# Kernel optimization log

Measured on AMD Instinct MI355X. Metric: run time of the kernel, lower is better.

## Reference

```python
import jax, jax.numpy as jnp
import numpy as np
from jax import lax

N = 20000          # num_nodes_total
N_GHOST = 2000     # nodes with mask == 0
T_IN = 8
FEAT = 16          # node_features
HID = 128          # hidden_dim
E = 320000         # edges (~avg degree 16)
D = 2              # downstream_concat_depth
ALPHA = 0.5        # alpha_boundary
FUSER_IN = FEAT * (1 + D) + 1   # 49
FUSER_H = max(32, 2 * FEAT * (1 + D))  # 96
GATE_H = max(8, FUSER_H // 2)   # 48


def _lin(k, fan_in, shape):
    b = 1.0 / np.sqrt(fan_in)
    return jax.random.uniform(k, shape, jnp.float32, -b, b)


def setup_inputs() -> dict:
    key = jax.random.key(0)
    ks = jax.random.split(key, 26)
    x = jax.random.normal(ks[0], (N, T_IN, FEAT), jnp.float32)
    src = jax.random.randint(ks[1], (E,), 0, N, jnp.int32)
    dst = jax.random.randint(ks[2], (E,), 0, N, jnp.int32)
    # guarantee every ghost node (ids [0, N_GHOST)) has an outgoing edge to a real node
    src = src.at[:N_GHOST].set(jnp.arange(N_GHOST, dtype=jnp.int32))
    dst = dst.at[:N_GHOST].set(jax.random.randint(ks[3], (N_GHOST,), N_GHOST, N, jnp.int32))
    edge_index = jnp.stack([src, dst])
    edge_attr = jax.random.uniform(ks[4], (E, 1), jnp.float32, minval=0.05, maxval=2.0)
    mask = jnp.concatenate([jnp.zeros(N_GHOST, jnp.int32), jnp.ones(N - N_GHOST, jnp.int32)])
    H3 = 3 * HID
    return dict(
        x=x, edge_attr=edge_attr,
        W_lin=_lin(ks[5], FEAT, (FEAT, HID)), b_lin=_lin(ks[6], FEAT, (HID,)),
        Wc1=_lin(ks[7], HID, (HID, HID)), bc1=jnp.zeros((HID,), jnp.float32),
        Wc2=_lin(ks[8], HID, (HID, HID)), bc2=jnp.zeros((HID,), jnp.float32),
        W_ih=_lin(ks[9], HID, (HID, H3)), b_ih=_lin(ks[10], HID, (H3,)),
        W_hh=_lin(ks[11], HID, (HID, H3)), b_hh=_lin(ks[12], HID, (H3,)),
        Wf1=_lin(ks[13], FUSER_IN, (FUSER_IN, FUSER_H)), bf1=_lin(ks[14], FUSER_IN, (FUSER_H,)),
        Wf2=_lin(ks[15], FUSER_H, (FUSER_H, FEAT)), bf2=_lin(ks[16], FUSER_H, (FEAT,)),
        Wg1=_lin(ks[17], FUSER_IN, (FUSER_IN, GATE_H)), bg1=_lin(ks[18], FUSER_IN, (GATE_H,)),
        Wg2=_lin(ks[19], GATE_H, (GATE_H, 1)), bg2=_lin(ks[20], GATE_H, (1,)),
        edge_index=edge_index, mask=mask,
    )


def _forward(x, edge_attr, W_lin, b_lin, Wc1, bc1, Wc2, bc2, W_ih, b_ih, W_hh, b_hh,
             Wf1, bf1, Wf2, bf2, Wg1, bg1, Wg2, bg2, edge_index, mask):
    src, dst = edge_index[0], edge_index[1]
    ghost_idx = jnp.nonzero(mask == 0, size=N_GHOST)[0]
    dist = jnp.maximum(edge_attr[:, 0], 1e-6)                     # [E]
    # first outgoing edge per source node (earliest edge id per src, cf. argsort trick)
    eid = jnp.arange(E, dtype=jnp.int32)
    first_eid = jax.ops.segment_min(eid, src, num_segments=N)    # int32 max where no edge
    has = first_eid < E
    safe = jnp.where(has, first_eid, 0)
    first_out = jnp.where(has, dst[safe], -1)                     # [N]
    first_dx = jnp.where(has, dist[safe], -1.0)                   # [N]
    b_idx = first_out[ghost_idx]                                  # boundary node per ghost
    dx_bnd = jnp.maximum(first_dx[ghost_idx], 1e-6)[:, None]      # [G,1]
    # D downstream hops, staying put where no outgoing edge exists
    dK, cur = [], b_idx
    for _ in range(D):
        nxt = first_out[cur]
        nxt = jnp.where(nxt < 0, cur, nxt)
        dK.append(nxt)
        cur = nxt
    # GCN symmetric normalization with self-loops (PyG gcn_norm)
    deg = jnp.zeros((N,), x.dtype).at[dst].add(1.0) + 1.0         # in-degree + self-loop
    dis = deg ** -0.5
    norm_e = (dis[src] * dis[dst])[:, None]                       # [E,1]
    norm_self = (1.0 / deg)[:, None]                              # [N,1]

    def gcn(h, W, b):
        hw = h @ W                                                # [N,HID]
        agg = jnp.zeros_like(hw).at[dst].add(hw[src] * norm_e)    # scatter-add messages
        return agg + hw * norm_self + b

    def gru(g, h):
        gi = g @ W_ih + b_ih                                      # [N,3H]
        gh = h @ W_hh + b_hh
        ir, iz, inn = jnp.split(gi, 3, axis=1)
        hr, hz, hn = jnp.split(gh, 3, axis=1)
        r = jax.nn.sigmoid(ir + hr)
        z = jax.nn.sigmoid(iz + hz)
        n = jnp.tanh(inn + r * hn)
        return (1.0 - z) * n + z * h

    def step(h, x_t):
        gf = x_t[ghost_idx]                                       # [G,F]
        feats = jnp.concatenate([gf] + [x_t[i] for i in dK] + [dx_bnd], axis=1)  # [G,FUSER_IN]
        zf = jax.nn.relu(feats @ Wf1 + bf1)
        delta = zf @ Wf2 + bf2
        gate = jax.nn.sigmoid(jax.nn.relu(feats @ Wg1 + bg1) @ Wg2 + bg2)
        x_t = x_t.at[ghost_idx].set(gf + ALPHA * delta * gate)
        g = jax.nn.relu(x_t @ W_lin + b_lin)
        g = jax.nn.relu(gcn(g, Wc1, bc1))
        g = jax.nn.relu(gcn(g, Wc2, bc2))
        return gru(g, h), None

    h0 = jnp.zeros((N, HID), x.dtype)
    h, _ = lax.scan(step, h0, jnp.swapaxes(x, 0, 1))              # scan over T_IN
    return h


def reference(x, edge_attr, W_lin, b_lin, Wc1, bc1, Wc2, bc2, W_ih, b_ih, W_hh, b_hh,
              Wf1, bf1, Wf2, bf2, Wg1, bg1, Wg2, bg2, edge_index, mask):
    return _forward(x, edge_attr, W_lin, b_lin, Wc1, bc1, Wc2, bc2, W_ih, b_ih, W_hh, b_hh,
                    Wf1, bf1, Wf2, bf2, Wg1, bg1, Wg2, bg2, edge_index, mask)
```

## Files before the change

### kernel.cpp

```cpp
#include <hip/hip_runtime.h>
#include <math.h>

#define NN 20000
#define T_IN 8
#define FEAT 16
#define HID 128
#define H3 384
#define FUSER_IN 49
#define FUSER_H 96
#define GATE_H 48
#define ALPHA 0.5f

typedef unsigned short u16;
typedef __attribute__((ext_vector_type(8))) short bf16x8_t;
typedef __attribute__((ext_vector_type(4))) float f32x4_t;

__device__ __forceinline__ float sigmoidf_(float v) { return 1.0f / (1.0f + expf(-v)); }

__device__ __forceinline__ u16 f2b(float v) {
    unsigned u = __float_as_uint(v);
    unsigned r = (u + 0x7fffu + ((u >> 16) & 1u)) >> 16;
    return (u16)r;
}
__device__ __forceinline__ float b2f(u16 u) { return __uint_as_float(((unsigned)u) << 16); }


__global__ void init_kernel(int* first_eid, int* deg_cnt, int* gcount, int n) {
    int i = blockIdx.x * 256 + threadIdx.x;
    if (i < n) { first_eid[i] = 0x7fffffff; deg_cnt[i] = 0; }
    if (i == 0) *gcount = 0;
}

__global__ void edge_pass1(const int* __restrict__ src, const int* __restrict__ dst,
                           int* first_eid, int* deg_cnt, int e) {
    int i = blockIdx.x * 256 + threadIdx.x;
    if (i < e) {
        atomicMin(&first_eid[src[i]], i);
        atomicAdd(&deg_cnt[dst[i]], 1);
    }
}

__global__ void scan1(const int* __restrict__ cnt, int* tmp, int* bsum, int n) {
    __shared__ int buf[256];
    int tid = threadIdx.x;
    int i = blockIdx.x * 256 + tid;
    int v = (i < n) ? cnt[i] : 0;
    buf[tid] = v;
    __syncthreads();
    #pragma unroll
    for (int off = 1; off < 256; off <<= 1) {
        int t = (tid >= off) ? buf[tid - off] : 0;
        __syncthreads();
        buf[tid] += t;
        __syncthreads();
    }
    if (i < n) tmp[i] = buf[tid];
    if (tid == 255) bsum[blockIdx.x] = buf[255];
}

__global__ void scan2(int* bsum, int nb) {
    __shared__ int buf[256];
    int tid = threadIdx.x;
    int v = (tid < nb) ? bsum[tid] : 0;
    buf[tid] = v;
    __syncthreads();
    #pragma unroll
    for (int off = 1; off < 256; off <<= 1) {
        int t = (tid >= off) ? buf[tid - off] : 0;
        __syncthreads();
        buf[tid] += t;
        __syncthreads();
    }
    if (tid < nb) bsum[tid] = buf[tid];
}

__global__ void scan3(const int* __restrict__ cnt, const int* __restrict__ tmp,
                      const int* __restrict__ bsum,
                      int* row_ptr, int* fill_ptr, float* dis, float* norm_self, int n) {
    int i = blockIdx.x * 256 + threadIdx.x;
    if (i >= n) return;
    int pre = (blockIdx.x > 0) ? bsum[blockIdx.x - 1] : 0;
    int incl = tmp[i] + pre;
    int v = cnt[i];
    row_ptr[i + 1] = incl;
    fill_ptr[i] = incl - v;
    float deg = (float)v + 1.0f;
    dis[i] = 1.0f / sqrtf(deg);
    norm_self[i] = 1.0f / deg;
    if (i == 0) row_ptr[0] = 0;
}

__global__ void firsts_kernel(const int* __restrict__ first_eid, const int* __restrict__ dst,
                              const float* __restrict__ edge_attr,
                              int* first_out, float* first_dx, int n, int e) {
    int i = blockIdx.x * 256 + threadIdx.x;
    if (i >= n) return;
    int fe = first_eid[i];
    if (fe < e) {
        first_out[i] = dst[fe];
        first_dx[i] = fmaxf(edge_attr[fe], 1e-6f);
    } else {
        first_out[i] = -1;
        first_dx[i] = -1.0f;
    }
}

__global__ void edge_pass2(const int* __restrict__ src, const int* __restrict__ dst,
                           int* fill_ptr, const float* __restrict__ dis,
                           int* csr_src, float* csr_w, int e) {
    int i = blockIdx.x * 256 + threadIdx.x;
    if (i < e) {
        int d = dst[i], s = src[i];
        int pos = atomicAdd(&fill_ptr[d], 1);
        csr_src[pos] = s;
        csr_w[pos] = dis[s] * dis[d];
    }
}

__global__ void ghost_kernel(const int* __restrict__ mask, const int* __restrict__ first_out,
                             const float* __restrict__ first_dx,
                             int* d1_of, int* d2_of, float* dxb_of,
                             int* ghost_list, int* ghost_pos, int* gcount, int n) {
    int i = blockIdx.x * 256 + threadIdx.x;
    if (i >= n) return;
    if (mask[i] != 0) { ghost_pos[i] = -1; return; }
    int pos = atomicAdd(gcount, 1);
    ghost_list[pos] = i;
    ghost_pos[i] = pos;
    int b = first_out[i];
    float dxb = fmaxf(first_dx[i], 1e-6f);
    int d1, d2;
    if (b < 0) { d1 = i; d2 = i; }
    else {
        int n1 = first_out[b]; d1 = (n1 < 0) ? b : n1;
        int n2 = first_out[d1]; d2 = (n2 < 0) ? d1 : n2;
    }
    d1_of[i] = d1; d2_of[i] = d2; dxb_of[i] = dxb;
}

__global__ void zero2_kernel(float* a, int na, unsigned* b, int nb) {
    int stride = gridDim.x * 256;
    for (int i = blockIdx.x * 256 + threadIdx.x; i < na; i += stride) a[i] = 0.0f;
    for (int i = blockIdx.x * 256 + threadIdx.x; i < nb; i += stride) b[i] = 0u;
}

__global__ __launch_bounds__(256)
void wsplit_kernel(const float* __restrict__ W, u16* BT_hi, u16* BT_lo, int Ncols) {
    __shared__ float tile[32][33];
    int nb = blockIdx.x * 32;
    int kb = blockIdx.y * 32;
    int tx = threadIdx.x & 31, ty = threadIdx.x >> 5;
    #pragma unroll
    for (int r = 0; r < 32; r += 8)
        tile[ty + r][tx] = W[(size_t)(kb + ty + r) * Ncols + nb + tx];
    __syncthreads();
    #pragma unroll
    for (int r = 0; r < 32; r += 8) {
        float v = tile[tx][ty + r];
        u16 h = f2b(v);
        size_t off = (size_t)(nb + ty + r) * 128 + kb + tx;
        BT_hi[off] = h;
        BT_lo[off] = f2b(v - b2f(h));
    }
}


__global__ __launch_bounds__(128)
void fuse_ghost(const float* __restrict__ x,
                const int* __restrict__ ghost_list, const int* __restrict__ gcount,
                const int* __restrict__ d1_of, const int* __restrict__ d2_of,
                const float* __restrict__ dxb_of,
                const float* __restrict__ Wf1, const float* __restrict__ bf1,
                const float* __restrict__ Wf2, const float* __restrict__ bf2,
                const float* __restrict__ Wg1, const float* __restrict__ bg1,
                const float* __restrict__ Wg2, const float* __restrict__ bg2,
                float* __restrict__ xf_buf) {
    int slot = blockIdx.x;
    if (slot >= *gcount) return;
    int t = blockIdx.y;
    int i = ghost_list[slot];
    int j = threadIdx.x;
    __shared__ float feats[FUSER_IN];
    __shared__ float z1[FUSER_H];
    __shared__ float zg[GATE_H];
    __shared__ float s_gate;

    if (j < FEAT) {
        int d1 = d1_of[i], d2 = d2_of[i];
        feats[j]            = x[((size_t)i * T_IN + t) * FEAT + j];
        feats[FEAT + j]     = x[((size_t)d1 * T_IN + t) * FEAT + j];
        feats[2 * FEAT + j] = x[((size_t)d2 * T_IN + t) * FEAT + j];
    }
    if (j == 0) feats[3 * FEAT] = dxb_of[i];
    __syncthreads();
    if (j < FUSER_H) {
        float acc = bf1[j];
        for (int k = 0; k < FUSER_IN; ++k) acc = fmaf(feats[k], Wf1[k * FUSER_H + j], acc);
        z1[j] = fmaxf(acc, 0.0f);
    }
    if (j < GATE_H) {
        float acc = bg1[j];
        for (int k = 0; k < FUSER_IN; ++k) acc = fmaf(feats[k], Wg1[k * GATE_H + j], acc);
        zg[j] = fmaxf(acc, 0.0f);
    }
    __syncthreads();
    if (j == 0) {
        float s = bg2[0];
        for (int k = 0; k < GATE_H; ++k) s = fmaf(zg[k], Wg2[k], s);
        s_gate = sigmoidf_(s);
    }
    __syncthreads();
    if (j < FEAT) {
        float acc = bf2[j];
        for (int k = 0; k < FUSER_H; ++k) acc = fmaf(z1[k], Wf2[k * FEAT + j], acc);
        xf_buf[((size_t)slot * T_IN + t) * FEAT + j] = feats[j] + ALPHA * acc * s_gate;
    }
}

__global__ __launch_bounds__(256)
void lin_all(const float* __restrict__ x, const float* __restrict__ xf_buf,
             const int* __restrict__ ghost_pos,
             const float* __restrict__ W_lin, const float* __restrict__ b_lin,
             u16* __restrict__ g8_hi, u16* __restrict__ g8_lo, int n, int total) {
    __shared__ float Wl[FEAT][HID];
    __shared__ float bl[HID];
    #pragma unroll
    for (int k8 = 0; k8 < 8; ++k8) {
        int idx = threadIdx.x + k8 * 256;
        Wl[idx >> 7][idx & 127] = W_lin[idx];
    }
    if (threadIdx.x < HID) bl[threadIdx.x] = b_lin[threadIdx.x];
    __syncthreads();
    int j = threadIdx.x & 127;
    for (int pair = blockIdx.x * 2 + (threadIdx.x >> 7); pair < total; pair += gridDim.x * 2) {
        int node = pair % n;
        int t = pair / n;
        int gp = ghost_pos[node];
        const float* xr = (gp >= 0) ? &xf_buf[((size_t)gp * T_IN + t) * FEAT]
                                    : &x[((size_t)node * T_IN + t) * FEAT];
        float acc = bl[j];
        #pragma unroll
        for (int k = 0; k < FEAT; ++k) acc = fmaf(xr[k], Wl[k][j], acc);
        float v = fmaxf(acc, 0.0f);
        u16 hv = f2b(v);
        size_t off = (size_t)pair * HID + j;
        g8_hi[off] = hv;
        g8_lo[off] = f2b(v - b2f(hv));
    }
}

__global__ __launch_bounds__(256)
void gemm_gcn_b(const u16* __restrict__ Ahi0, const u16* __restrict__ Alo0,
                const u16* __restrict__ BThi, const u16* __restrict__ BTlo,
                u16* __restrict__ Cb0, int M) {
    constexpr int BM = 64;
    __shared__ u16 ldsA[2][BM * 128];
    const size_t tOff = (size_t)blockIdx.z * M * 128;
    const u16* Ahi = Ahi0 + tOff;
    const u16* Alo = Alo0 + tOff;
    u16*       Cb  = Cb0 + tOff;

    const int tid  = threadIdx.x;
    const int row0 = blockIdx.x * BM;
    constexpr int MF = BM / 32;

    #pragma unroll
    for (int it = 0; it < BM / 16; ++it) {
        int unit = tid + it * 256;
        int r = unit >> 4, s = unit & 15;
        int gr = row0 + r;
        uint4 vh = make_uint4(0, 0, 0, 0), vl = vh;
        if (gr < M) {
            vh = *reinterpret_cast<const uint4*>(&Ahi[(size_t)gr * 128 + s * 8]);
            vl = *reinterpret_cast<const uint4*>(&Alo[(size_t)gr * 128 + s * 8]);
        }
        int byte = (r * 256 + s * 16) ^ ((r & 7) << 4);
        *reinterpret_cast<uint4*>((char*)(&ldsA[0][0]) + byte) = vh;
        *reinterpret_cast<uint4*>((char*)(&ldsA[1][0]) + byte) = vl;
    }
    __syncthreads();

    const int wid  = tid >> 6;
    const int lane = tid & 63;
    const int wr = (wid >> 1) * (BM / 2);
    const int wc = (wid & 1) * 64;
    const int l15 = lane & 15;
    const int lkh = lane >> 4;

    f32x4_t acc[MF][4] = {};

    #pragma unroll
    for (int kb = 0; kb < 4; ++kb) {
        bf16x8_t ah[MF], al[MF], bh[4], bl[4];
        #pragma unroll
        for (int m = 0; m < MF; ++m) {
            int row = wr + m * 16 + l15;
            int byte = (row * 256 + kb * 64 + lkh * 16) ^ ((row & 7) << 4);
            ah[m] = *reinterpret_cast<const bf16x8_t*>((const char*)(&ldsA[0][0]) + byte);
            al[m] = *reinterpret_cast<const bf16x8_t*>((const char*)(&ldsA[1][0]) + byte);
        }
        #pragma unroll
        for (int nf = 0; nf < 4; ++nf) {
            int col = wc + nf * 16 + l15;
            size_t off = (size_t)col * 128 + kb * 32 + lkh * 8;
            bh[nf] = *reinterpret_cast<const bf16x8_t*>(&BThi[off]);
            bl[nf] = *reinterpret_cast<const bf16x8_t*>(&BTlo[off]);
        }
        #pragma unroll
        for (int m = 0; m < MF; ++m)
            #pragma unroll
            for (int nf = 0; nf < 4; ++nf) {
                acc[m][nf] = __builtin_amdgcn_mfma_f32_16x16x32_bf16(ah[m], bh[nf], acc[m][nf], 0, 0, 0);
                acc[m][nf] = __builtin_amdgcn_mfma_f32_16x16x32_bf16(ah[m], bl[nf], acc[m][nf], 0, 0, 0);
                acc[m][nf] = __builtin_amdgcn_mfma_f32_16x16x32_bf16(al[m], bh[nf], acc[m][nf], 0, 0, 0);
            }
    }

    #pragma unroll
    for (int m = 0; m < MF; ++m) {
        int rbase = row0 + wr + m * 16 + lkh * 4;
        #pragma unroll
        for (int nf = 0; nf < 4; ++nf) {
            int col = wc + nf * 16 + l15;
            #pragma unroll
            for (int r2 = 0; r2 < 4; ++r2) {
                int row = rbase + r2;
                if (row < M) Cb[(size_t)row * 128 + col] = f2b(acc[m][nf][r2]);
            }
        }
    }
}

__global__ __launch_bounds__(256)
void gcn_agg_b(const u16* __restrict__ hwb0,
               const int* __restrict__ row_ptr,
               const int* __restrict__ csr_src, const float* __restrict__ csr_w,
               const float* __restrict__ norm_self, const float* __restrict__ bias,
               u16* __restrict__ g_hi0, u16* __restrict__ g_lo0, int n) {
    int t   = blockIdx.x & 7;
    int blk = blockIdx.x >> 3;
    int node = blk * 8 + (threadIdx.x >> 5);
    int lane = threadIdx.x & 31;
    if (node >= n) return;
    const size_t tOff = (size_t)t * n * 128;
    const u16* hwb = hwb0 + tOff;
    u16* g_hi = g_hi0 + tOff;
    u16* g_lo = g_lo0 + tOff;

    ushort4 sv = *reinterpret_cast<const ushort4*>(&hwb[(size_t)node * HID + lane * 4]);
    float ns = norm_self[node];
    float4 a0, a1, a2, a3;
    a0.x = b2f(sv.x) * ns; a0.y = b2f(sv.y) * ns; a0.z = b2f(sv.z) * ns; a0.w = b2f(sv.w) * ns;
    a1 = make_float4(0.f, 0.f, 0.f, 0.f); a2 = a1; a3 = a1;
    int p  = row_ptr[node];
    int p1 = row_ptr[node + 1];
    for (; p + 4 <= p1; p += 4) {
        int s0 = csr_src[p], s1 = csr_src[p + 1], s2 = csr_src[p + 2], s3 = csr_src[p + 3];
        float w0 = csr_w[p], w1 = csr_w[p + 1], w2 = csr_w[p + 2], w3 = csr_w[p + 3];
        ushort4 v0 = *reinterpret_cast<const ushort4*>(&hwb[(size_t)s0 * HID + lane * 4]);
        ushort4 v1 = *reinterpret_cast<const ushort4*>(&hwb[(size_t)s1 * HID + lane * 4]);
        ushort4 v2 = *reinterpret_cast<const ushort4*>(&hwb[(size_t)s2 * HID + lane * 4]);
        ushort4 v3 = *reinterpret_cast<const ushort4*>(&hwb[(size_t)s3 * HID + lane * 4]);
        a0.x = fmaf(b2f(v0.x), w0, a0.x); a0.y = fmaf(b2f(v0.y), w0, a0.y);
        a0.z = fmaf(b2f(v0.z), w0, a0.z); a0.w = fmaf(b2f(v0.w), w0, a0.w);
        a1.x = fmaf(b2f(v1.x), w1, a1.x); a1.y = fmaf(b2f(v1.y), w1, a1.y);
        a1.z = fmaf(b2f(v1.z), w1, a1.z); a1.w = fmaf(b2f(v1.w), w1, a1.w);
        a2.x = fmaf(b2f(v2.x), w2, a2.x); a2.y = fmaf(b2f(v2.y), w2, a2.y);
        a2.z = fmaf(b2f(v2.z), w2, a2.z); a2.w = fmaf(b2f(v2.w), w2, a2.w);
        a3.x = fmaf(b2f(v3.x), w3, a3.x); a3.y = fmaf(b2f(v3.y), w3, a3.y);
        a3.z = fmaf(b2f(v3.z), w3, a3.z); a3.w = fmaf(b2f(v3.w), w3, a3.w);
    }
    for (; p < p1; ++p) {
        int s = csr_src[p];
        float w = csr_w[p];
        ushort4 v = *reinterpret_cast<const ushort4*>(&hwb[(size_t)s * HID + lane * 4]);
        a0.x = fmaf(b2f(v.x), w, a0.x); a0.y = fmaf(b2f(v.y), w, a0.y);
        a0.z = fmaf(b2f(v.z), w, a0.z); a0.w = fmaf(b2f(v.w), w, a0.w);
    }
    float4 b4 = reinterpret_cast<const float4*>(bias)[lane];
    float ox = fmaxf(a0.x + a1.x + a2.x + a3.x + b4.x, 0.0f);
    float oy = fmaxf(a0.y + a1.y + a2.y + a3.y + b4.y, 0.0f);
    float oz = fmaxf(a0.z + a1.z + a2.z + a3.z + b4.z, 0.0f);
    float ow = fmaxf(a0.w + a1.w + a2.w + a3.w + b4.w, 0.0f);
    ushort4 hv, lv;
    hv.x = f2b(ox); lv.x = f2b(ox - b2f(hv.x));
    hv.y = f2b(oy); lv.y = f2b(oy - b2f(hv.y));
    hv.z = f2b(oz); lv.z = f2b(oz - b2f(hv.z));
    hv.w = f2b(ow); lv.w = f2b(ow - b2f(hv.w));
    *reinterpret_cast<ushort4*>(&g_hi[(size_t)node * HID + lane * 4]) = hv;
    *reinterpret_cast<ushort4*>(&g_lo[(size_t)node * HID + lane * 4]) = lv;
}


__global__ __launch_bounds__(256)
void gemm_gru(const u16* __restrict__ Ahi1, const u16* __restrict__ Alo1,
              const u16* __restrict__ BThi1, const u16* __restrict__ BTlo1,
              float* __restrict__ C1,
              const u16* __restrict__ Ahi2, const u16* __restrict__ Alo2,
              const u16* __restrict__ BThi2, const u16* __restrict__ BTlo2,
              float* __restrict__ C2,
              int M, int Ncols) {
    constexpr int BM = 128;
    __shared__ u16 ldsA[2][BM * 128];
    const u16* Ahi  = blockIdx.z ? Ahi2  : Ahi1;
    const u16* Alo  = blockIdx.z ? Alo2  : Alo1;
    const u16* BThi = blockIdx.z ? BThi2 : BThi1;
    const u16* BTlo = blockIdx.z ? BTlo2 : BTlo1;
    float*     C    = blockIdx.z ? C2    : C1;

    const int tid  = threadIdx.x;
    const int row0 = blockIdx.x * BM;
    const int col0 = blockIdx.y * 128;
    constexpr int MF = BM / 32;

    #pragma unroll
    for (int it = 0; it < BM / 16; ++it) {
        int unit = tid + it * 256;
        int r = unit >> 4, s = unit & 15;
        int gr = row0 + r;
        uint4 vh = make_uint4(0, 0, 0, 0), vl = vh;
        if (gr < M) {
            vh = *reinterpret_cast<const uint4*>(&Ahi[(size_t)gr * 128 + s * 8]);
            vl = *reinterpret_cast<const uint4*>(&Alo[(size_t)gr * 128 + s * 8]);
        }
        int byte = (r * 256 + s * 16) ^ ((r & 7) << 4);
        *reinterpret_cast<uint4*>((char*)(&ldsA[0][0]) + byte) = vh;
        *reinterpret_cast<uint4*>((char*)(&ldsA[1][0]) + byte) = vl;
    }
    __syncthreads();

    const int wid  = tid >> 6;
    const int lane = tid & 63;
    const int wr = (wid >> 1) * (BM / 2);
    const int wc = (wid & 1) * 64;
    const int l15 = lane & 15;
    const int lkh = lane >> 4;

    f32x4_t acc[MF][4] = {};

    #pragma unroll
    for (int kb = 0; kb < 4; ++kb) {
        bf16x8_t ah[MF], al[MF], bh[4], bl[4];
        #pragma unroll
        for (int m = 0; m < MF; ++m) {
            int row = wr + m * 16 + l15;
            int byte = (row * 256 + kb * 64 + lkh * 16) ^ ((row & 7) << 4);
            ah[m] = *reinterpret_cast<const bf16x8_t*>((const char*)(&ldsA[0][0]) + byte);
            al[m] = *reinterpret_cast<const bf16x8_t*>((const char*)(&ldsA[1][0]) + byte);
        }
        #pragma unroll
        for (int nf = 0; nf < 4; ++nf) {
            int col = col0 + wc + nf * 16 + l15;
            size_t off = (size_t)col * 128 + kb * 32 + lkh * 8;
            bh[nf] = *reinterpret_cast<const bf16x8_t*>(&BThi[off]);
            bl[nf] = *reinterpret_cast<const bf16x8_t*>(&BTlo[off]);
        }
        #pragma unroll
        for (int m = 0; m < MF; ++m)
            #pragma unroll
            for (int nf = 0; nf < 4; ++nf) {
                acc[m][nf] = __builtin_amdgcn_mfma_f32_16x16x32_bf16(ah[m], bh[nf], acc[m][nf], 0, 0, 0);
                acc[m][nf] = __builtin_amdgcn_mfma_f32_16x16x32_bf16(ah[m], bl[nf], acc[m][nf], 0, 0, 0);
                acc[m][nf] = __builtin_amdgcn_mfma_f32_16x16x32_bf16(al[m], bh[nf], acc[m][nf], 0, 0, 0);
            }
    }

    #pragma unroll
    for (int m = 0; m < MF; ++m) {
        int rbase = row0 + wr + m * 16 + lkh * 4;
        #pragma unroll
        for (int nf = 0; nf < 4; ++nf) {
            int col = col0 + wc + nf * 16 + l15;
            #pragma unroll
            for (int r2 = 0; r2 < 4; ++r2) {
                int row = rbase + r2;
                if (row < M) C[(size_t)row * Ncols + col] = acc[m][nf][r2];
            }
        }
    }
}

__global__ __launch_bounds__(256)
void gru_kernel(const float* __restrict__ gi, const float* __restrict__ gh,
                const float* __restrict__ b_ih, const float* __restrict__ b_hh,
                float* __restrict__ h, u16* __restrict__ h_hi, u16* __restrict__ h_lo, int n) {
    int idx = blockIdx.x * 256 + threadIdx.x;
    if (idx >= n * 32) return;
    int row = idx >> 5, q = idx & 31;
    const float4* gi4 = reinterpret_cast<const float4*>(gi + (size_t)row * H3);
    const float4* gh4 = reinterpret_cast<const float4*>(gh + (size_t)row * H3);
    const float4* bi4 = reinterpret_cast<const float4*>(b_ih);
    const float4* bh4 = reinterpret_cast<const float4*>(b_hh);
    float4 vir = gi4[q], viz = gi4[32 + q], vin = gi4[64 + q];
    float4 vhr = gh4[q], vhz = gh4[32 + q], vhn = gh4[64 + q];
    float4 bir = bi4[q], biz = bi4[32 + q], bin_ = bi4[64 + q];
    float4 bhr = bh4[q], bhz = bh4[32 + q], bhn = bh4[64 + q];
    float4* h4 = reinterpret_cast<float4*>(h);
    float4 hv = h4[idx];
    float4 o;
    {
        float r = sigmoidf_((vir.x + bir.x) + (vhr.x + bhr.x));
        float z = sigmoidf_((viz.x + biz.x) + (vhz.x + bhz.x));
        float nn2 = tanhf((vin.x + bin_.x) + r * (vhn.x + bhn.x));
        o.x = (1.0f - z) * nn2 + z * hv.x;
    }
    {
        float r = sigmoidf_((vir.y + bir.y) + (vhr.y + bhr.y));
        float z = sigmoidf_((viz.y + biz.y) + (vhz.y + bhz.y));
        float nn2 = tanhf((vin.y + bin_.y) + r * (vhn.y + bhn.y));
        o.y = (1.0f - z) * nn2 + z * hv.y;
    }
    {
        float r = sigmoidf_((vir.z + bir.z) + (vhr.z + bhr.z));
        float z = sigmoidf_((viz.z + biz.z) + (vhz.z + bhz.z));
        float nn2 = tanhf((vin.z + bin_.z) + r * (vhn.z + bhn.z));
        o.z = (1.0f - z) * nn2 + z * hv.z;
    }
    {
        float r = sigmoidf_((vir.w + bir.w) + (vhr.w + bhr.w));
        float z = sigmoidf_((viz.w + biz.w) + (vhz.w + bhz.w));
        float nn2 = tanhf((vin.w + bin_.w) + r * (vhn.w + bhn.w));
        o.w = (1.0f - z) * nn2 + z * hv.w;
    }
    h4[idx] = o;
    ushort4 hvv, lvv;
    hvv.x = f2b(o.x); lvv.x = f2b(o.x - b2f(hvv.x));
    hvv.y = f2b(o.y); lvv.y = f2b(o.y - b2f(hvv.y));
    hvv.z = f2b(o.z); lvv.z = f2b(o.z - b2f(hvv.z));
    hvv.w = f2b(o.w); lvv.w = f2b(o.w - b2f(hvv.w));
    *reinterpret_cast<ushort4*>(&h_hi[(size_t)row * HID + q * 4]) = hvv;
    *reinterpret_cast<ushort4*>(&h_lo[(size_t)row * HID + q * 4]) = lvv;
}


extern "C" void kernel_launch(void* const* d_in, const int* in_sizes, int n_in,
                              void* d_out, int out_size, void* d_ws, size_t ws_size,
                              hipStream_t stream) {
    const float* x        = (const float*)d_in[0];
    const float* edge_attr= (const float*)d_in[1];
    const float* W_lin    = (const float*)d_in[2];
    const float* b_lin    = (const float*)d_in[3];
    const float* Wc1      = (const float*)d_in[4];
    const float* bc1      = (const float*)d_in[5];
    const float* Wc2      = (const float*)d_in[6];
    const float* bc2      = (const float*)d_in[7];
    const float* W_ih     = (const float*)d_in[8];
    const float* b_ih     = (const float*)d_in[9];
    const float* W_hh     = (const float*)d_in[10];
    const float* b_hh     = (const float*)d_in[11];
    const float* Wf1      = (const float*)d_in[12];
    const float* bf1      = (const float*)d_in[13];
    const float* Wf2      = (const float*)d_in[14];
    const float* bf2      = (const float*)d_in[15];
    const float* Wg1      = (const float*)d_in[16];
    const float* bg1      = (const float*)d_in[17];
    const float* Wg2      = (const float*)d_in[18];
    const float* bg2      = (const float*)d_in[19];
    const int*   edge_index = (const int*)d_in[20];
    const int*   mask     = (const int*)d_in[21];

    const int n = in_sizes[21];
    const int e = in_sizes[1];
    const int* src = edge_index;
    const int* dst = edge_index + e;
    float* h = (float*)d_out;

    char* w = (char*)d_ws;
    auto alloc = [&](size_t bytes) -> char* {
        char* p = w;
        w += (bytes + 255) & ~(size_t)255;
        return p;
    };
    int*   first_eid = (int*)  alloc((size_t)n * 4);
    int*   deg_cnt   = (int*)  alloc((size_t)n * 4);
    int*   row_ptr   = (int*)  alloc((size_t)(n + 1) * 4);
    int*   fill_ptr  = (int*)  alloc((size_t)n * 4);
    int*   tmp_scan  = (int*)  alloc((size_t)n * 4);
    int*   bsum      = (int*)  alloc((size_t)256 * 4);
    float* dis       = (float*)alloc((size_t)n * 4);
    float* norm_self = (float*)alloc((size_t)n * 4);
    int*   first_out = (int*)  alloc((size_t)n * 4);
    float* first_dx  = (float*)alloc((size_t)n * 4);
    int*   d1_of     = (int*)  alloc((size_t)n * 4);
    int*   d2_of     = (int*)  alloc((size_t)n * 4);
    float* dxb_of    = (float*)alloc((size_t)n * 4);
    int*   ghost_list= (int*)  alloc((size_t)n * 4);
    int*   ghost_pos = (int*)  alloc((size_t)n * 4);
    int*   gcount    = (int*)  alloc(256);
    int*   csr_src   = (int*)  alloc((size_t)e * 4);
    float* csr_w     = (float*)alloc((size_t)e * 4);
    u16* Wc1T_hi = (u16*)alloc((size_t)HID * 128 * 2);
    u16* Wc1T_lo = (u16*)alloc((size_t)HID * 128 * 2);
    u16* Wc2T_hi = (u16*)alloc((size_t)HID * 128 * 2);
    u16* Wc2T_lo = (u16*)alloc((size_t)HID * 128 * 2);
    u16* WihT_hi = (u16*)alloc((size_t)H3 * 128 * 2);
    u16* WihT_lo = (u16*)alloc((size_t)H3 * 128 * 2);
    u16* WhhT_hi = (u16*)alloc((size_t)H3 * 128 * 2);
    u16* WhhT_lo = (u16*)alloc((size_t)H3 * 128 * 2);
    u16*   g8_hi = (u16*)  alloc((size_t)T_IN * n * HID * 2);
    u16*   g8_lo = (u16*)  alloc((size_t)T_IN * n * HID * 2);
    u16*   bufHb = (u16*)  alloc((size_t)T_IN * n * HID * 2);
    float* bufGi = (float*)alloc((size_t)n * H3 * 4);
    float* bufGh = (float*)alloc((size_t)n * H3 * 4);
    float* xf_buf= (float*)alloc((size_t)n * T_IN * FEAT * 4);
    u16*   h_hi  = (u16*)  alloc((size_t)n * HID * 2);
    u16*   h_lo  = (u16*)  alloc((size_t)n * HID * 2);

    const int TPB = 256;
    const int nb = (n + 255) / 256;
    dim3 gN(nb), gE((e + TPB - 1) / TPB);

    init_kernel<<<gN, TPB, 0, stream>>>(first_eid, deg_cnt, gcount, n);
    edge_pass1<<<gE, TPB, 0, stream>>>(src, dst, first_eid, deg_cnt, e);
    scan1<<<gN, TPB, 0, stream>>>(deg_cnt, tmp_scan, bsum, n);
    scan2<<<1, TPB, 0, stream>>>(bsum, nb);
    scan3<<<gN, TPB, 0, stream>>>(deg_cnt, tmp_scan, bsum, row_ptr, fill_ptr, dis, norm_self, n);
    firsts_kernel<<<gN, TPB, 0, stream>>>(first_eid, dst, edge_attr, first_out, first_dx, n, e);
    edge_pass2<<<gE, TPB, 0, stream>>>(src, dst, fill_ptr, dis, csr_src, csr_w, e);
    ghost_kernel<<<gN, TPB, 0, stream>>>(mask, first_out, first_dx, d1_of, d2_of, dxb_of,
                                         ghost_list, ghost_pos, gcount, n);
    wsplit_kernel<<<dim3(HID / 32, 4), TPB, 0, stream>>>(Wc1, Wc1T_hi, Wc1T_lo, HID);
    wsplit_kernel<<<dim3(HID / 32, 4), TPB, 0, stream>>>(Wc2, Wc2T_hi, Wc2T_lo, HID);
    wsplit_kernel<<<dim3(H3 / 32, 4), TPB, 0, stream>>>(W_ih, WihT_hi, WihT_lo, H3);
    wsplit_kernel<<<dim3(H3 / 32, 4), TPB, 0, stream>>>(W_hh, WhhT_hi, WhhT_lo, H3);

    zero2_kernel<<<2048, TPB, 0, stream>>>(h, n * HID, (unsigned*)h_hi, n * HID);

    fuse_ghost<<<dim3(n, T_IN), 128, 0, stream>>>(x, ghost_list, gcount, d1_of, d2_of, dxb_of,
                                                  Wf1, bf1, Wf2, bf2, Wg1, bg1, Wg2, bg2,
                                                  xf_buf);
    lin_all<<<2048, 256, 0, stream>>>(x, xf_buf, ghost_pos, W_lin, b_lin,
                                      g8_hi, g8_lo, n, n * T_IN);
    dim3 grid_gcn((n + 63) / 64, 1, T_IN);
    const int agg_blocks = ((n + 7) / 8) * T_IN;
    gemm_gcn_b<<<grid_gcn, 256, 0, stream>>>(g8_hi, g8_lo, Wc1T_hi, Wc1T_lo, bufHb, n);
    gcn_agg_b<<<agg_blocks, 256, 0, stream>>>(bufHb, row_ptr, csr_src, csr_w,
                                              norm_self, bc1, g8_hi, g8_lo, n);
    gemm_gcn_b<<<grid_gcn, 256, 0, stream>>>(g8_hi, g8_lo, Wc2T_hi, Wc2T_lo, bufHb, n);
    gcn_agg_b<<<agg_blocks, 256, 0, stream>>>(bufHb, row_ptr, csr_src, csr_w,
                                              norm_self, bc2, g8_hi, g8_lo, n);

    dim3 grid_gru((n + 127) / 128, 3, 2);
    for (int t = 0; t < T_IN; ++t) {
        const u16* Gt_hi = g8_hi + (size_t)t * n * HID;
        const u16* Gt_lo = g8_lo + (size_t)t * n * HID;
        gemm_gru<<<grid_gru, 256, 0, stream>>>(
            Gt_hi, Gt_lo, WihT_hi, WihT_lo, bufGi,
            h_hi, h_lo, WhhT_hi, WhhT_lo, bufGh, n, H3);
        gru_kernel<<<(n * 32 + TPB - 1) / TPB, TPB, 0, stream>>>(bufGi, bufGh, b_ih, b_hh,
                                                                 h, h_hi, h_lo, n);
    }
}
```

Baseline: 938.0 us.

## Fuse GRU gate GEMMs with the elementwise update and split GCN aggregation by columns

The separate GRU GEMM kernel, which wrote fp32 gate pre-activations for the input and hidden paths to global buffers, and the elementwise GRU kernel that read them back are replaced by one kernel. Each block loads a 32-row tile of the input and hidden state into LDS, computes all three gates for both paths with split-bf16 MFMA, and applies the GRU update in registers. This removes the large per-timestep round trip through the gate buffers, at the cost of each block re-reading the full weight matrices from cache. The GCN aggregation kernel now handles 16 nodes per block with 16 lanes each, and splits the feature columns into two halves across separate blocks, which doubles the block count and shortens each lane's work.

```diff
diff --git a/kernel.cpp b/kernel.cpp
--- a/kernel.cpp
+++ b/kernel.cpp
@@ -336,18 +336,22 @@
                const int* __restrict__ row_ptr,
                const int* __restrict__ csr_src, const float* __restrict__ csr_w,
                const float* __restrict__ norm_self, const float* __restrict__ bias,
-               u16* __restrict__ g_hi0, u16* __restrict__ g_lo0, int n) {
-    int t   = blockIdx.x & 7;
-    int blk = blockIdx.x >> 3;
-    int node = blk * 8 + (threadIdx.x >> 5);
-    int lane = threadIdx.x & 31;
+               u16* __restrict__ g_hi0, u16* __restrict__ g_lo0, int n, int nblk) {
+    int bid = blockIdx.x;
+    int t = bid & 7;
+    int q = bid >> 3;
+    int blk = q % nblk;
+    int half = q / nblk;
+    int node = blk * 16 + (threadIdx.x >> 4);
+    int lane = threadIdx.x & 15;
     if (node >= n) return;
     const size_t tOff = (size_t)t * n * 128;
     const u16* hwb = hwb0 + tOff;
     u16* g_hi = g_hi0 + tOff;
     u16* g_lo = g_lo0 + tOff;
-
-    ushort4 sv = *reinterpret_cast<const ushort4*>(&hwb[(size_t)node * HID + lane * 4]);
+    const int cb = half * 64 + lane * 4;
+
+    ushort4 sv = *reinterpret_cast<const ushort4*>(&hwb[(size_t)node * HID + cb]);
     float ns = norm_self[node];
     float4 a0, a1, a2, a3;
     a0.x = b2f(sv.x) * ns; a0.y = b2f(sv.y) * ns; a0.z = b2f(sv.z) * ns; a0.w = b2f(sv.w) * ns;
@@ -357,10 +361,10 @@
     for (; p + 4 <= p1; p += 4) {
         int s0 = csr_src[p], s1 = csr_src[p + 1], s2 = csr_src[p + 2], s3 = csr_src[p + 3];
         float w0 = csr_w[p], w1 = csr_w[p + 1], w2 = csr_w[p + 2], w3 = csr_w[p + 3];
-        ushort4 v0 = *reinterpret_cast<const ushort4*>(&hwb[(size_t)s0 * HID + lane * 4]);
-        ushort4 v1 = *reinterpret_cast<const ushort4*>(&hwb[(size_t)s1 * HID + lane * 4]);
-        ushort4 v2 = *reinterpret_cast<const ushort4*>(&hwb[(size_t)s2 * HID + lane * 4]);
-        ushort4 v3 = *reinterpret_cast<const ushort4*>(&hwb[(size_t)s3 * HID + lane * 4]);
+        ushort4 v0 = *reinterpret_cast<const ushort4*>(&hwb[(size_t)s0 * HID + cb]);
+        ushort4 v1 = *reinterpret_cast<const ushort4*>(&hwb[(size_t)s1 * HID + cb]);
+        ushort4 v2 = *reinterpret_cast<const ushort4*>(&hwb[(size_t)s2 * HID + cb]);
+        ushort4 v3 = *reinterpret_cast<const ushort4*>(&hwb[(size_t)s3 * HID + cb]);
         a0.x = fmaf(b2f(v0.x), w0, a0.x); a0.y = fmaf(b2f(v0.y), w0, a0.y);
         a0.z = fmaf(b2f(v0.z), w0, a0.z); a0.w = fmaf(b2f(v0.w), w0, a0.w);
         a1.x = fmaf(b2f(v1.x), w1, a1.x); a1.y = fmaf(b2f(v1.y), w1, a1.y);
@@ -373,11 +377,11 @@
     for (; p < p1; ++p) {
         int s = csr_src[p];
         float w = csr_w[p];
-        ushort4 v = *reinterpret_cast<const ushort4*>(&hwb[(size_t)s * HID + lane * 4]);
+        ushort4 v = *reinterpret_cast<const ushort4*>(&hwb[(size_t)s * HID + cb]);
         a0.x = fmaf(b2f(v.x), w, a0.x); a0.y = fmaf(b2f(v.y), w, a0.y);
         a0.z = fmaf(b2f(v.z), w, a0.z); a0.w = fmaf(b2f(v.w), w, a0.w);
     }
-    float4 b4 = reinterpret_cast<const float4*>(bias)[lane];
+    float4 b4 = reinterpret_cast<const float4*>(bias)[half * 16 + lane];
     float ox = fmaxf(a0.x + a1.x + a2.x + a3.x + b4.x, 0.0f);
     float oy = fmaxf(a0.y + a1.y + a2.y + a3.y + b4.y, 0.0f);
     float oz = fmaxf(a0.z + a1.z + a2.z + a3.z + b4.z, 0.0f);
@@ -387,149 +391,111 @@
     hv.y = f2b(oy); lv.y = f2b(oy - b2f(hv.y));
     hv.z = f2b(oz); lv.z = f2b(oz - b2f(hv.z));
     hv.w = f2b(ow); lv.w = f2b(ow - b2f(hv.w));
-    *reinterpret_cast<ushort4*>(&g_hi[(size_t)node * HID + lane * 4]) = hv;
-    *reinterpret_cast<ushort4*>(&g_lo[(size_t)node * HID + lane * 4]) = lv;
+    *reinterpret_cast<ushort4*>(&g_hi[(size_t)node * HID + cb]) = hv;
+    *reinterpret_cast<ushort4*>(&g_lo[(size_t)node * HID + cb]) = lv;
 }
 
 
 __global__ __launch_bounds__(256)
-void gemm_gru(const u16* __restrict__ Ahi1, const u16* __restrict__ Alo1,
-              const u16* __restrict__ BThi1, const u16* __restrict__ BTlo1,
-              float* __restrict__ C1,
-              const u16* __restrict__ Ahi2, const u16* __restrict__ Alo2,
-              const u16* __restrict__ BThi2, const u16* __restrict__ BTlo2,
-              float* __restrict__ C2,
-              int M, int Ncols) {
-    constexpr int BM = 128;
-    __shared__ u16 ldsA[2][BM * 128];
-    const u16* Ahi  = blockIdx.z ? Ahi2  : Ahi1;
-    const u16* Alo  = blockIdx.z ? Alo2  : Alo1;
-    const u16* BThi = blockIdx.z ? BThi2 : BThi1;
-    const u16* BTlo = blockIdx.z ? BTlo2 : BTlo1;
-    float*     C    = blockIdx.z ? C2    : C1;
-
+void gru_fused2(const u16* __restrict__ g_hi, const u16* __restrict__ g_lo,
+                const u16* __restrict__ h_hi, const u16* __restrict__ h_lo,
+                const u16* __restrict__ WihT_hi, const u16* __restrict__ WihT_lo,
+                const u16* __restrict__ WhhT_hi, const u16* __restrict__ WhhT_lo,
+                const float* __restrict__ b_ih, const float* __restrict__ b_hh,
+                float* __restrict__ h, u16* __restrict__ h_hi_o, u16* __restrict__ h_lo_o,
+                int n) {
+    __shared__ u16 lds[4][32 * 128];
     const int tid  = threadIdx.x;
-    const int row0 = blockIdx.x * BM;
-    const int col0 = blockIdx.y * 128;
-    constexpr int MF = BM / 32;
-
-    #pragma unroll
-    for (int it = 0; it < BM / 16; ++it) {
+    const int row0 = blockIdx.x * 32;
+
+    #pragma unroll
+    for (int it = 0; it < 2; ++it) {
         int unit = tid + it * 256;
         int r = unit >> 4, s = unit & 15;
         int gr = row0 + r;
-        uint4 vh = make_uint4(0, 0, 0, 0), vl = vh;
-        if (gr < M) {
-            vh = *reinterpret_cast<const uint4*>(&Ahi[(size_t)gr * 128 + s * 8]);
-            vl = *reinterpret_cast<const uint4*>(&Alo[(size_t)gr * 128 + s * 8]);
+        uint4 vg = make_uint4(0,0,0,0), vG = vg, vh = vg, vH = vg;
+        if (gr < n) {
+            size_t goff = (size_t)gr * 128 + s * 8;
+            vg = *reinterpret_cast<const uint4*>(&g_hi[goff]);
+            vG = *reinterpret_cast<const uint4*>(&g_lo[goff]);
+            vh = *reinterpret_cast<const uint4*>(&h_hi[goff]);
+            vH = *reinterpret_cast<const uint4*>(&h_lo[goff]);
         }
         int byte = (r * 256 + s * 16) ^ ((r & 7) << 4);
-        *reinterpret_cast<uint4*>((char*)(&ldsA[0][0]) + byte) = vh;
-        *reinterpret_cast<uint4*>((char*)(&ldsA[1][0]) + byte) = vl;
+        *reinterpret_cast<uint4*>((char*)(&lds[0][0]) + byte) = vg;
+        *reinterpret_cast<uint4*>((char*)(&lds[1][0]) + byte) = vG;
+        *reinterpret_cast<uint4*>((char*)(&lds[2][0]) + byte) = vh;
+        *reinterpret_cast<uint4*>((char*)(&lds[3][0]) + byte) = vH;
     }
     __syncthreads();
 
     const int wid  = tid >> 6;
     const int lane = tid & 63;
-    const int wr = (wid >> 1) * (BM / 2);
-    const int wc = (wid & 1) * 64;
-    const int l15 = lane & 15;
-    const int lkh = lane >> 4;
-
-    f32x4_t acc[MF][4] = {};
+    const int l15  = lane & 15;
+    const int lkh  = lane >> 4;
+
+    f32x4_t agi[3][2][2] = {};
+    f32x4_t agh[3][2][2] = {};
 
     #pragma unroll
     for (int kb = 0; kb < 4; ++kb) {
-        bf16x8_t ah[MF], al[MF], bh[4], bl[4];
-        #pragma unroll
-        for (int m = 0; m < MF; ++m) {
-            int row = wr + m * 16 + l15;
+        bf16x8_t Agh[2], Agl[2], Ahh[2], Ahl[2];
+        #pragma unroll
+        for (int m = 0; m < 2; ++m) {
+            int row = m * 16 + l15;
             int byte = (row * 256 + kb * 64 + lkh * 16) ^ ((row & 7) << 4);
-            ah[m] = *reinterpret_cast<const bf16x8_t*>((const char*)(&ldsA[0][0]) + byte);
-            al[m] = *reinterpret_cast<const bf16x8_t*>((const char*)(&ldsA[1][0]) + byte);
-        }
-        #pragma unroll
-        for (int nf = 0; nf < 4; ++nf) {
-            int col = col0 + wc + nf * 16 + l15;
-            size_t off = (size_t)col * 128 + kb * 32 + lkh * 8;
-            bh[nf] = *reinterpret_cast<const bf16x8_t*>(&BThi[off]);
-            bl[nf] = *reinterpret_cast<const bf16x8_t*>(&BTlo[off]);
-        }
-        #pragma unroll
-        for (int m = 0; m < MF; ++m)
+            Agh[m] = *reinterpret_cast<const bf16x8_t*>((const char*)(&lds[0][0]) + byte);
+            Agl[m] = *reinterpret_cast<const bf16x8_t*>((const char*)(&lds[1][0]) + byte);
+            Ahh[m] = *reinterpret_cast<const bf16x8_t*>((const char*)(&lds[2][0]) + byte);
+            Ahl[m] = *reinterpret_cast<const bf16x8_t*>((const char*)(&lds[3][0]) + byte);
+        }
+        #pragma unroll
+        for (int gt = 0; gt < 3; ++gt) {
             #pragma unroll
-            for (int nf = 0; nf < 4; ++nf) {
-                acc[m][nf] = __builtin_amdgcn_mfma_f32_16x16x32_bf16(ah[m], bh[nf], acc[m][nf], 0, 0, 0);
-                acc[m][nf] = __builtin_amdgcn_mfma_f32_16x16x32_bf16(ah[m], bl[nf], acc[m][nf], 0, 0, 0);
-                acc[m][nf] = __builtin_amdgcn_mfma_f32_16x16x32_bf16(al[m], bh[nf], acc[m][nf], 0, 0, 0);
+            for (int nf = 0; nf < 2; ++nf) {
+                int col = gt * HID + wid * 32 + nf * 16 + l15;
+                size_t off = (size_t)col * 128 + kb * 32 + lkh * 8;
+                bf16x8_t bih = *reinterpret_cast<const bf16x8_t*>(&WihT_hi[off]);
+                bf16x8_t bil = *reinterpret_cast<const bf16x8_t*>(&WihT_lo[off]);
+                bf16x8_t bhh = *reinterpret_cast<const bf16x8_t*>(&WhhT_hi[off]);
+                bf16x8_t bhl = *reinterpret_cast<const bf16x8_t*>(&WhhT_lo[off]);
+                #pragma unroll
+                for (int m = 0; m < 2; ++m) {
+                    agi[gt][m][nf] = __builtin_amdgcn_mfma_f32_16x16x32_bf16(Agh[m], bih, agi[gt][m][nf], 0, 0, 0);
+                    agi[gt][m][nf] = __builtin_amdgcn_mfma_f32_16x16x32_bf16(Agh[m], bil, agi[gt][m][nf], 0, 0, 0);
+                    agi[gt][m][nf] = __builtin_amdgcn_mfma_f32_16x16x32_bf16(Agl[m], bih, agi[gt][m][nf], 0, 0, 0);
+                    agh[gt][m][nf] = __builtin_amdgcn_mfma_f32_16x16x32_bf16(Ahh[m], bhh, agh[gt][m][nf], 0, 0, 0);
+                    agh[gt][m][nf] = __builtin_amdgcn_mfma_f32_16x16x32_bf16(Ahh[m], bhl, agh[gt][m][nf], 0, 0, 0);
+                    agh[gt][m][nf] = __builtin_amdgcn_mfma_f32_16x16x32_bf16(Ahl[m], bhh, agh[gt][m][nf], 0, 0, 0);
+                }
             }
-    }
-
-    #pragma unroll
-    for (int m = 0; m < MF; ++m) {
-        int rbase = row0 + wr + m * 16 + lkh * 4;
-        #pragma unroll
-        for (int nf = 0; nf < 4; ++nf) {
-            int col = col0 + wc + nf * 16 + l15;
+        }
+    }
+
+    #pragma unroll
+    for (int nf = 0; nf < 2; ++nf) {
+        int col = wid * 32 + nf * 16 + l15;
+        float bir = b_ih[col], biz = b_ih[HID + col], bin_ = b_ih[2 * HID + col];
+        float bhr = b_hh[col], bhz = b_hh[HID + col], bhn = b_hh[2 * HID + col];
+        #pragma unroll
+        for (int m = 0; m < 2; ++m) {
             #pragma unroll
             for (int r2 = 0; r2 < 4; ++r2) {
-                int row = rbase + r2;
-                if (row < M) C[(size_t)row * Ncols + col] = acc[m][nf][r2];
+                int grow = row0 + m * 16 + lkh * 4 + r2;
+                if (grow >= n) continue;
+                float rr = sigmoidf_((agi[0][m][nf][r2] + bir) + (agh[0][m][nf][r2] + bhr));
+                float zz = sigmoidf_((agi[1][m][nf][r2] + biz) + (agh[1][m][nf][r2] + bhz));
+                float nn2 = tanhf((agi[2][m][nf][r2] + bin_) + rr * (agh[2][m][nf][r2] + bhn));
+                size_t off = (size_t)grow * HID + col;
+                float hold = h[off];
+                float hnew = (1.0f - zz) * nn2 + zz * hold;
+                h[off] = hnew;
+                u16 hv = f2b(hnew);
+                h_hi_o[off] = hv;
+                h_lo_o[off] = f2b(hnew - b2f(hv));
             }
         }
     }
-}
-
-__global__ __launch_bounds__(256)
-void gru_kernel(const float* __restrict__ gi, const float* __restrict__ gh,
-                const float* __restrict__ b_ih, const float* __restrict__ b_hh,
-                float* __restrict__ h, u16* __restrict__ h_hi, u16* __restrict__ h_lo, int n) {
-    int idx = blockIdx.x * 256 + threadIdx.x;
-    if (idx >= n * 32) return;
-    int row = idx >> 5, q = idx & 31;
-    const float4* gi4 = reinterpret_cast<const float4*>(gi + (size_t)row * H3);
-    const float4* gh4 = reinterpret_cast<const float4*>(gh + (size_t)row * H3);
-    const float4* bi4 = reinterpret_cast<const float4*>(b_ih);
-    const float4* bh4 = reinterpret_cast<const float4*>(b_hh);
-    float4 vir = gi4[q], viz = gi4[32 + q], vin = gi4[64 + q];
-    float4 vhr = gh4[q], vhz = gh4[32 + q], vhn = gh4[64 + q];
-    float4 bir = bi4[q], biz = bi4[32 + q], bin_ = bi4[64 + q];
-    float4 bhr = bh4[q], bhz = bh4[32 + q], bhn = bh4[64 + q];
-    float4* h4 = reinterpret_cast<float4*>(h);
-    float4 hv = h4[idx];
-    float4 o;
-    {
-        float r = sigmoidf_((vir.x + bir.x) + (vhr.x + bhr.x));
-        float z = sigmoidf_((viz.x + biz.x) + (vhz.x + bhz.x));
-        float nn2 = tanhf((vin.x + bin_.x) + r * (vhn.x + bhn.x));
-        o.x = (1.0f - z) * nn2 + z * hv.x;
-    }
-    {
-        float r = sigmoidf_((vir.y + bir.y) + (vhr.y + bhr.y));
-        float z = sigmoidf_((viz.y + biz.y) + (vhz.y + bhz.y));
-        float nn2 = tanhf((vin.y + bin_.y) + r * (vhn.y + bhn.y));
-        o.y = (1.0f - z) * nn2 + z * hv.y;
-    }
-    {
-        float r = sigmoidf_((vir.z + bir.z) + (vhr.z + bhr.z));
-        float z = sigmoidf_((viz.z + biz.z) + (vhz.z + bhz.z));
-        float nn2 = tanhf((vin.z + bin_.z) + r * (vhn.z + bhn.z));
-        o.z = (1.0f - z) * nn2 + z * hv.z;
-    }
-    {
-        float r = sigmoidf_((vir.w + bir.w) + (vhr.w + bhr.w));
-        float z = sigmoidf_((viz.w + biz.w) + (vhz.w + bhz.w));
-        float nn2 = tanhf((vin.w + bin_.w) + r * (vhn.w + bhn.w));
-        o.w = (1.0f - z) * nn2 + z * hv.w;
-    }
-    h4[idx] = o;
-    ushort4 hvv, lvv;
-    hvv.x = f2b(o.x); lvv.x = f2b(o.x - b2f(hvv.x));
-    hvv.y = f2b(o.y); lvv.y = f2b(o.y - b2f(hvv.y));
-    hvv.z = f2b(o.z); lvv.z = f2b(o.z - b2f(hvv.z));
-    hvv.w = f2b(o.w); lvv.w = f2b(o.w - b2f(hvv.w));
-    *reinterpret_cast<ushort4*>(&h_hi[(size_t)row * HID + q * 4]) = hvv;
-    *reinterpret_cast<ushort4*>(&h_lo[(size_t)row * HID + q * 4]) = lvv;
 }
 
 
@@ -600,8 +566,6 @@
     u16*   g8_hi = (u16*)  alloc((size_t)T_IN * n * HID * 2);
     u16*   g8_lo = (u16*)  alloc((size_t)T_IN * n * HID * 2);
     u16*   bufHb = (u16*)  alloc((size_t)T_IN * n * HID * 2);
-    float* bufGi = (float*)alloc((size_t)n * H3 * 4);
-    float* bufGh = (float*)alloc((size_t)n * H3 * 4);
     float* xf_buf= (float*)alloc((size_t)n * T_IN * FEAT * 4);
     u16*   h_hi  = (u16*)  alloc((size_t)n * HID * 2);
     u16*   h_lo  = (u16*)  alloc((size_t)n * HID * 2);
@@ -632,22 +596,21 @@
     lin_all<<<2048, 256, 0, stream>>>(x, xf_buf, ghost_pos, W_lin, b_lin,
                                       g8_hi, g8_lo, n, n * T_IN);
     dim3 grid_gcn((n + 63) / 64, 1, T_IN);
-    const int agg_blocks = ((n + 7) / 8) * T_IN;
+    const int nblk16 = (n + 15) / 16;
+    const int agg_blocks = 2 * 8 * nblk16;
     gemm_gcn_b<<<grid_gcn, 256, 0, stream>>>(g8_hi, g8_lo, Wc1T_hi, Wc1T_lo, bufHb, n);
     gcn_agg_b<<<agg_blocks, 256, 0, stream>>>(bufHb, row_ptr, csr_src, csr_w,
-                                              norm_self, bc1, g8_hi, g8_lo, n);
+                                              norm_self, bc1, g8_hi, g8_lo, n, nblk16);
     gemm_gcn_b<<<grid_gcn, 256, 0, stream>>>(g8_hi, g8_lo, Wc2T_hi, Wc2T_lo, bufHb, n);
     gcn_agg_b<<<agg_blocks, 256, 0, stream>>>(bufHb, row_ptr, csr_src, csr_w,
-                                              norm_self, bc2, g8_hi, g8_lo, n);
-
-    dim3 grid_gru((n + 127) / 128, 3, 2);
+                                              norm_self, bc2, g8_hi, g8_lo, n, nblk16);
+
+    const int gru_blocks = (n + 31) / 32;
     for (int t = 0; t < T_IN; ++t) {
         const u16* Gt_hi = g8_hi + (size_t)t * n * HID;
         const u16* Gt_lo = g8_lo + (size_t)t * n * HID;
-        gemm_gru<<<grid_gru, 256, 0, stream>>>(
-            Gt_hi, Gt_lo, WihT_hi, WihT_lo, bufGi,
-            h_hi, h_lo, WhhT_hi, WhhT_lo, bufGh, n, H3);
-        gru_kernel<<<(n * 32 + TPB - 1) / TPB, TPB, 0, stream>>>(bufGi, bufGh, b_ih, b_hh,
-                                                                 h, h_hi, h_lo, n);
-    }
-}
+        gru_fused2<<<gru_blocks, 256, 0, stream>>>(Gt_hi, Gt_lo, h_hi, h_lo,
+                                                   WihT_hi, WihT_lo, WhhT_hi, WhhT_lo,
+                                                   b_ih, b_hh, h, h_hi, h_lo, n);
+    }
+}
```

New measurement: 952.7 us. About the same (+1.6%).
